# Optimization experiments

Measured on AMD Instinct MI355X. Metric: run time of the kernel, lower is better.

## Reference

```python
import jax, jax.numpy as jnp
import numpy as np

V, D, B, L = 100000, 64, 4096, 200

def setup_inputs() -> dict:
    key = jax.random.key(0)
    ks = jax.random.split(key, 10)
    s = 0.05  # keep activations in a sane range for sigmoid
    return {
        "item_ids": jax.random.randint(ks[0], (B,), 0, V),
        "history": jax.random.randint(ks[1], (B, L), 0, V),
        "hist_len": jax.random.randint(ks[2], (B,), 1, L + 1),
        "emb_table": jax.random.normal(ks[3], (V, D), jnp.float32) * s,
        "aW1": jax.random.normal(ks[4], (3 * D, D), jnp.float32) * s,
        "ab1": jnp.zeros((D,), jnp.float32),
        "aW2": jax.random.normal(ks[5], (D, 1), jnp.float32) * s,
        "ab2": jnp.zeros((1,), jnp.float32),
        "fW1": jax.random.normal(ks[6], (3 * D, 128), jnp.float32) * s,
        "fb1": jnp.zeros((128,), jnp.float32),
        "fW2": jax.random.normal(ks[7], (128, 64), jnp.float32) * s,
        "fb2": jnp.zeros((64,), jnp.float32),
        "fW3": jax.random.normal(ks[8], (64, 1), jnp.float32) * s,
        "fb3": jnp.zeros((1,), jnp.float32),
    }

def reference(item_ids, history, hist_len, emb_table, aW1, ab1, aW2, ab2,
              fW1, fb1, fW2, fb2, fW3, fb3):
    target = emb_table[item_ids]                      # [B, D]
    hist = emb_table[history]                         # [B, L, D]
    # original pads short histories with zero rows -> zero the padded tail
    mask = (jnp.arange(hist.shape[1])[None, :] < hist_len[:, None]).astype(hist.dtype)
    hist = hist * mask[..., None]
    tgt = jnp.broadcast_to(target[:, None, :], hist.shape)     # [B, L, D]
    # attention_fc takes 3*D features: (hist, target, hist*target)
    feat = jnp.concatenate([hist, tgt, hist * tgt], axis=-1)   # [B, L, 3D]
    h = jax.nn.relu(feat @ aW1 + ab1)                 # [B, L, D]
    scores = (h @ aW2 + ab2)[..., 0]                  # [B, L]
    # faithful to original: softmax over full padded length (no length mask)
    w = jax.nn.softmax(scores, axis=1)
    pooled = jnp.einsum('bl,bld->bd', w, hist)        # [B, D]
    comb = jnp.concatenate([target, pooled, pooled - target], axis=-1)  # [B, 3D]
    z = jax.nn.relu(comb @ fW1 + fb1)
    z = jax.nn.relu(z @ fW2 + fb2)
    return jax.nn.sigmoid(z @ fW3 + fb3)              # [B, 1]
```

## Files before the change

### kernel.cpp

```cpp
#include <hip/hip_runtime.h>
#include <hip/hip_bf16.h>

#define NV 100000
#define ND 64
#define NB 4096
#define NL 200
#define MT 13

typedef __bf16 bf16_t;
typedef __bf16 bf16x8 __attribute__((ext_vector_type(8)));
typedef __bf16 bf16x4 __attribute__((ext_vector_type(4)));
typedef float f32x4 __attribute__((ext_vector_type(4)));

#define TB_ELEMS ((long)NV * ND)
#define TBV (TB_ELEMS / 8)
#define FT1 (128 * 192)
#define FT2 (64 * 128)
#define AWT (64 * 192)
#define CVT_TASKS (TBV + FT1 + FT2 + AWT)

__global__ __launch_bounds__(256)
void cvt_kernel(const float* __restrict__ emb,
                const float* __restrict__ aW1,
                const float* __restrict__ fW1,
                const float* __restrict__ fW2,
                bf16_t* __restrict__ tb,
                bf16_t* __restrict__ fW1T,
                bf16_t* __restrict__ fW2T,
                bf16_t* __restrict__ awT)
{
    long t = (long)blockIdx.x * 256 + threadIdx.x;
    if (t >= CVT_TASKS) return;
    if (t < TBV) {
        long i = t * 8;
        f32x4 a0 = *(const f32x4*)(emb + i);
        f32x4 a1 = *(const f32x4*)(emb + i + 4);
        bf16x8 o;
#pragma unroll
        for (int j = 0; j < 4; ++j) { o[j] = (bf16_t)a0[j]; o[j + 4] = (bf16_t)a1[j]; }
        *(bf16x8*)(tb + i) = o;
    } else {
        int u = (int)(t - TBV);
        if (u < FT1) {
            int n = u / 192, k = u - n * 192;
            fW1T[u] = (bf16_t)fW1[k * 128 + n];
        } else if (u < FT1 + FT2) {
            int u2 = u - FT1;
            int n = u2 >> 7, k = u2 & 127;
            fW2T[u2] = (bf16_t)fW2[k * 64 + n];
        } else {
            int u3 = u - FT1 - FT2;
            int n = u3 / 192, k = u3 - n * 192;
            awT[u3] = (bf16_t)aW1[k * 64 + n];
        }
    }
}

__global__ __launch_bounds__(512, 4)
void din_kernel1(const int* __restrict__ item_ids,
                 const int* __restrict__ history,
                 const int* __restrict__ hist_len,
                 const float* __restrict__ emb,
                 const bf16_t* __restrict__ tb,
                 const bf16_t* __restrict__ awT,
                 const float* __restrict__ ab1,
                 const float* __restrict__ aW2,
                 const bf16_t* __restrict__ fW1T, const float* __restrict__ fb1,
                 const bf16_t* __restrict__ fW2T, const float* __restrict__ fb2,
                 const float* __restrict__ fW3, const float* __restrict__ fb3,
                 float* __restrict__ out)
{
    __shared__ __align__(16) bf16_t histA[2][208 * 64];
    __shared__ __align__(16) bf16_t wbT[2][64 * 64];
    __shared__ float tgt[2][64];
    __shared__ __align__(16) float scores[2][208];
    __shared__ float wts[2][208];
    __shared__ float pp2[2][512];
    __shared__ float red[2][8];
    __shared__ float cb2[2][64];

    bf16_t* comb16 = (bf16_t*)wbT;
    bf16_t* z1s    = (bf16_t*)wbT + 3200;
    float*  z2f    = (float*)((bf16_t*)wbT + 5376);

    const int b0  = blockIdx.x * 2;
    const int tid = threadIdx.x;
    const int len0 = hist_len[b0];
    const int len1 = hist_len[b0 + 1];

    if (tid < 128) {
        int bx = tid >> 6, d = tid & 63;
        tgt[bx][d] = emb[(long)item_ids[b0 + bx] * ND + d];
    }

    {
        const int p = tid & 1;
        const int s = tid >> 1;
        const int bxA = (s >= 208);
        const int lA  = s - bxA * 208;
        const int lB  = s + 48;
        const int lenA = bxA ? len1 : len0;
        const bool vB = (s < 160);
        const bf16x8 z = (bf16x8)(bf16_t)0.f;
        bf16x8 a0 = z, a1 = z, a2 = z, a3 = z;
        bf16x8 c0 = z, c1 = z, c2 = z, c3 = z;
        if (lA < lenA) {
            const bf16_t* src = tb + (long)history[(long)(b0 + bxA) * NL + lA] * ND + p * 32;
            a0 = *(const bf16x8*)(src);
            a1 = *(const bf16x8*)(src + 8);
            a2 = *(const bf16x8*)(src + 16);
            a3 = *(const bf16x8*)(src + 24);
        }
        if (vB && lB < len1) {
            const bf16_t* src = tb + (long)history[(long)(b0 + 1) * NL + lB] * ND + p * 32;
            c0 = *(const bf16x8*)(src);
            c1 = *(const bf16x8*)(src + 8);
            c2 = *(const bf16x8*)(src + 16);
            c3 = *(const bf16x8*)(src + 24);
        }
        {
            bf16_t* d = &histA[bxA][lA * 64];
            const int S = (lA & 7) << 3;
            *(bf16x8*)&d[(p * 32 +  0) ^ S] = a0;
            *(bf16x8*)&d[(p * 32 +  8) ^ S] = a1;
            *(bf16x8*)&d[(p * 32 + 16) ^ S] = a2;
            *(bf16x8*)&d[(p * 32 + 24) ^ S] = a3;
        }
        if (vB) {
            bf16_t* d = &histA[1][lB * 64];
            const int S = (lB & 7) << 3;
            *(bf16x8*)&d[(p * 32 +  0) ^ S] = c0;
            *(bf16x8*)&d[(p * 32 +  8) ^ S] = c1;
            *(bf16x8*)&d[(p * 32 + 16) ^ S] = c2;
            *(bf16x8*)&d[(p * 32 + 24) ^ S] = c3;
        }
    }

    {
        const int n  = tid & 63;
        const int kp = tid >> 6;
        const long t0 = (long)item_ids[b0] * ND;
        const long t1 = (long)item_ids[b0 + 1] * ND;
        f32x4 tk0a = *(const f32x4*)(emb + t0 + kp * 8);
        f32x4 tk0b = *(const f32x4*)(emb + t0 + kp * 8 + 4);
        f32x4 tk1a = *(const f32x4*)(emb + t1 + kp * 8);
        f32x4 tk1b = *(const f32x4*)(emb + t1 + kp * 8 + 4);
        bf16x8 va = *(const bf16x8*)&awT[n * 192 + kp * 8];
        bf16x8 vm = *(const bf16x8*)&awT[n * 192 + 64 + kp * 8];
        bf16x8 vp = *(const bf16x8*)&awT[n * 192 + 128 + kp * 8];
        float cs0 = 0.f, cs1 = 0.f;
        bf16x8 w0v, w1v;
#pragma unroll
        for (int i = 0; i < 8; ++i) {
            float tk0 = (i < 4) ? tk0a[i] : tk0b[i - 4];
            float tk1 = (i < 4) ? tk1a[i] : tk1b[i - 4];
            float ah = (float)va[i];
            float am = (float)vm[i];
            float ap = (float)vp[i];
            w0v[i] = (bf16_t)(ah + tk0 * ap);
            w1v[i] = (bf16_t)(ah + tk1 * ap);
            cs0 += tk0 * am;
            cs1 += tk1 * am;
        }
        const int S = (n & 7) << 3;
        *(bf16x8*)&wbT[0][n * 64 + ((kp * 8) ^ S)] = w0v;
        *(bf16x8*)&wbT[1][n * 64 + ((kp * 8) ^ S)] = w1v;
        pp2[0][kp * 64 + n] = cs0;
        pp2[1][kp * 64 + n] = cs1;
    }
    __syncthreads();

    if (tid < 128) {
        const int bx = tid >> 6, n = tid & 63;
        float s = ab1[n];
#pragma unroll
        for (int kp = 0; kp < 8; ++kp) s += pp2[bx][kp * 64 + n];
        cb2[bx][n] = s;
    }
    __syncthreads();

    {
        const int wave = tid >> 6;
        const int lane = tid & 63;
        const int bx   = wave & 1;
        const int col  = lane & 15;
        const int quad = lane >> 4;

        bf16x8 afrag[4][2];
#pragma unroll
        for (int nt = 0; nt < 4; ++nt) {
            const int n = nt * 16 + col;
            const int S = (n & 7) << 3;
#pragma unroll
            for (int kb = 0; kb < 2; ++kb)
                afrag[nt][kb] = *(const bf16x8*)&wbT[bx][n * 64 + ((kb * 32 + quad * 8) ^ S)];
        }
        float cv[4][4], a2[4][4];
#pragma unroll
        for (int nt = 0; nt < 4; ++nt)
#pragma unroll
            for (int i = 0; i < 4; ++i) {
                const int no = nt * 16 + quad * 4 + i;
                cv[nt][i] = cb2[bx][no];
                a2[nt][i] = aW2[no];
            }

        for (int mt = (wave >> 1); mt < MT; mt += 4) {
            const int l = mt * 16 + col;
            const int S = (l & 7) << 3;
            const bf16_t* base = &histA[bx][l * 64];
            bf16x8 bf0 = *(const bf16x8*)&base[(     quad * 8) ^ S];
            bf16x8 bf1 = *(const bf16x8*)&base[(32 + quad * 8) ^ S];
            float sc = 0.f;
#pragma unroll
            for (int nt = 0; nt < 4; ++nt) {
                f32x4 acc = {cv[nt][0], cv[nt][1], cv[nt][2], cv[nt][3]};
                acc = __builtin_amdgcn_mfma_f32_16x16x32_bf16(afrag[nt][0], bf0, acc, 0, 0, 0);
                acc = __builtin_amdgcn_mfma_f32_16x16x32_bf16(afrag[nt][1], bf1, acc, 0, 0, 0);
#pragma unroll
                for (int i = 0; i < 4; ++i) {
                    float h = acc[i] > 0.f ? acc[i] : 0.f;
                    sc += h * a2[nt][i];
                }
            }
            sc += __shfl_xor(sc, 16, 64);
            sc += __shfl_xor(sc, 32, 64);
            if (quad == 0) scores[bx][mt * 16 + col] = sc;
        }
    }
    __syncthreads();

    {
        const int bx = tid >> 8, t = tid & 255;
        float s = (t < NL) ? scores[bx][t] : -1e30f;
        float m = s;
        for (int off = 32; off > 0; off >>= 1) m = fmaxf(m, __shfl_xor(m, off, 64));
        float e = (t < NL) ? __expf(s - m) : 0.f;
        if (t < NL) wts[bx][t] = e;
        else if (t < 208) wts[bx][t] = 0.f;
        float ss = e;
        for (int off = 32; off > 0; off >>= 1) ss += __shfl_xor(ss, off, 64);
        if ((t & 63) == 0) { red[bx][t >> 6] = m; red[bx][4 + (t >> 6)] = ss; }
    }
    __syncthreads();

    {
        const int bx = tid >> 8, t = tid & 255;
        const int c = t & 15;
        const int g = t >> 4;
        const int w4 = (tid >> 6) & 3;
        const float m0 = red[bx][0], m1 = red[bx][1], m2 = red[bx][2], m3 = red[bx][3];
        const float mg = fmaxf(fmaxf(m0, m1), fmaxf(m2, m3));
        float sc0 = __expf(m0 - mg), sc1 = __expf(m1 - mg);
        float sc2 = __expf(m2 - mg), sc3 = __expf(m3 - mg);
        const float rtot = 1.f / (sc0 * red[bx][4] + sc1 * red[bx][5] +
                                  sc2 * red[bx][6] + sc3 * red[bx][7]);
        sc0 *= rtot; sc1 *= rtot; sc2 *= rtot; sc3 *= rtot;
        f32x4 acc = {0.f, 0.f, 0.f, 0.f};
#pragma unroll
        for (int j = 0; j < 13; ++j) {
            const int l = g + j * 16;
            const float scj = (j < 4) ? sc0 : (j < 8) ? sc1 : (j < 12) ? sc2 : sc3;
            const float wl = wts[bx][l] * scj;
            bf16x4 v = *(const bf16x4*)&histA[bx][l * 64 + ((c * 4) ^ ((l & 7) << 3))];
#pragma unroll
            for (int k = 0; k < 4; ++k) acc[k] += wl * (float)v[k];
        }
#pragma unroll
        for (int k = 0; k < 4; ++k) {
            acc[k] += __shfl_xor(acc[k], 16, 64);
            acc[k] += __shfl_xor(acc[k], 32, 64);
        }
        if ((tid & 63) < 16) *(f32x4*)&pp2[bx][w4 * 64 + c * 4] = acc;
    }

    bf16x8 bw1[6]; float b1v;
    bf16x8 bw2[4]; float b2v = 0.f;
    {
        const int wave = tid >> 6, lane = tid & 63;
        const int col = lane & 15, quad = lane >> 4;
        const int n = wave * 16 + col;
#pragma unroll
        for (int ks = 0; ks < 6; ++ks)
            bw1[ks] = *(const bf16x8*)&fW1T[(long)n * 192 + ks * 32 + quad * 8];
        b1v = fb1[n];
        if (wave < 4) {
            const int n2 = wave * 16 + col;
#pragma unroll
            for (int ks = 0; ks < 4; ++ks)
                bw2[ks] = *(const bf16x8*)&fW2T[(long)n2 * 128 + ks * 32 + quad * 8];
            b2v = fb2[n2];
        }
    }
    __syncthreads();

    {
        const int bx = tid >> 8, t = tid & 255;
        if (t < 192) {
            const int d = t & 63;
            float v;
            if (t < 64) v = tgt[bx][d];
            else {
                float pl = pp2[bx][d] + pp2[bx][64 + d] + pp2[bx][128 + d] + pp2[bx][192 + d];
                v = (t < 128) ? pl : pl - tgt[bx][d];
            }
            comb16[bx * 200 + t] = (bf16_t)v;
        }
        if (tid >= 384) {
            const bf16x8 z = (bf16x8)(bf16_t)0.f;
            const int u = tid - 384;
#pragma unroll
            for (int s = u; s < 350; s += 128) *(bf16x8*)&comb16[400 + s * 8] = z;
        }
    }
    __syncthreads();

    {
        const int wave = tid >> 6, lane = tid & 63;
        const int col = lane & 15, quad = lane >> 4;
        f32x4 acc = {b1v, b1v, b1v, b1v};
#pragma unroll
        for (int ks = 0; ks < 6; ++ks) {
            bf16x8 a = *(const bf16x8*)&comb16[col * 200 + ks * 32 + quad * 8];
            acc = __builtin_amdgcn_mfma_f32_16x16x32_bf16(a, bw1[ks], acc, 0, 0, 0);
        }
        const int n = wave * 16 + col;
#pragma unroll
        for (int i = 0; i < 4; ++i) {
            const int m = quad * 4 + i;
            float zv = (m < 2) ? fmaxf(acc[i], 0.f) : 0.f;
            z1s[m * 136 + n] = (bf16_t)zv;
        }
    }
    __syncthreads();

    {
        const int wave = tid >> 6, lane = tid & 63;
        const int col = lane & 15, quad = lane >> 4;
        if (wave < 4) {
            f32x4 acc = {b2v, b2v, b2v, b2v};
#pragma unroll
            for (int ks = 0; ks < 4; ++ks) {
                bf16x8 a = *(const bf16x8*)&z1s[col * 136 + ks * 32 + quad * 8];
                acc = __builtin_amdgcn_mfma_f32_16x16x32_bf16(a, bw2[ks], acc, 0, 0, 0);
            }
            const int n2 = wave * 16 + col;
#pragma unroll
            for (int i = 0; i < 4; ++i) {
                const int m = quad * 4 + i;
                if (m < 2) z2f[m * 64 + n2] = fmaxf(acc[i], 0.f);
            }
        }
    }
    __syncthreads();

    if (tid < 128) {
        const int bx = tid >> 6, j = tid & 63;
        float s = z2f[bx * 64 + j] * fW3[j];
        for (int off = 32; off > 0; off >>= 1) s += __shfl_xor(s, off, 64);
        if (j == 0) out[b0 + bx] = 1.f / (1.f + __expf(-(s + fb3[0])));
    }
}

extern "C" void kernel_launch(void* const* d_in, const int* in_sizes, int n_in,
                              void* d_out, int out_size, void* d_ws, size_t ws_size,
                              hipStream_t stream) {
    const int*   item_ids = (const int*)d_in[0];
    const int*   history  = (const int*)d_in[1];
    const int*   hist_len = (const int*)d_in[2];
    const float* emb      = (const float*)d_in[3];
    const float* aW1      = (const float*)d_in[4];
    const float* ab1      = (const float*)d_in[5];
    const float* aW2      = (const float*)d_in[6];
    const float* fW1      = (const float*)d_in[8];
    const float* fb1      = (const float*)d_in[9];
    const float* fW2      = (const float*)d_in[10];
    const float* fb2      = (const float*)d_in[11];
    const float* fW3      = (const float*)d_in[12];
    const float* fb3      = (const float*)d_in[13];

    bf16_t* tb   = (bf16_t*)d_ws;
    bf16_t* fW1T = tb + TB_ELEMS;
    bf16_t* fW2T = fW1T + FT1;
    bf16_t* awTp = fW2T + FT2;

    cvt_kernel<<<(int)((CVT_TASKS + 255) / 256), 256, 0, stream>>>(
        emb, aW1, fW1, fW2, tb, fW1T, fW2T, awTp);
    din_kernel1<<<NB / 2, 512, 0, stream>>>(item_ids, history, hist_len, emb, tb,
                                            awTp, ab1, aW2,
                                            fW1T, fb1, fW2T, fb2, fW3, fb3,
                                            (float*)d_out);
}
```

Before: 145.1 us.

## Restructure target-weight folding, drop padding zeroing, and hoist MLP weight loads

The folded attention-weight setup now gives each wave a single batch element and reduces the target-dependent bias with wave shuffles. This removes the shared-memory partial-sum pass and one block barrier. aW1 is converted to bf16 without a transpose, so the conversion writes are coalesced, and the kernel reads it row-wise. The fW1/fW2 register loads are moved ahead of the pooling step so their latency overlaps it. The zero-fill of unused comb16/z1s rows is removed, so those MFMA rows hold stale data whose results are then discarded.

```diff
diff --git a/kernel.cpp b/kernel.cpp
--- a/kernel.cpp
+++ b/kernel.cpp
@@ -16,8 +16,8 @@
 #define TBV (TB_ELEMS / 8)
 #define FT1 (128 * 192)
 #define FT2 (64 * 128)
-#define AWT (64 * 192)
-#define CVT_TASKS (TBV + FT1 + FT2 + AWT)
+#define AWB (192 * 64)
+#define CVT_TASKS (TBV + FT1 + FT2 + AWB)
 
 __global__ __launch_bounds__(256)
 void cvt_kernel(const float* __restrict__ emb,
@@ -27,7 +27,7 @@
                 bf16_t* __restrict__ tb,
                 bf16_t* __restrict__ fW1T,
                 bf16_t* __restrict__ fW2T,
-                bf16_t* __restrict__ awT)
+                bf16_t* __restrict__ awB)
 {
     long t = (long)blockIdx.x * 256 + threadIdx.x;
     if (t >= CVT_TASKS) return;
@@ -50,8 +50,7 @@
             fW2T[u2] = (bf16_t)fW2[k * 64 + n];
         } else {
             int u3 = u - FT1 - FT2;
-            int n = u3 / 192, k = u3 - n * 192;
-            awT[u3] = (bf16_t)aW1[k * 64 + n];
+            awB[u3] = (bf16_t)aW1[u3];
         }
     }
 }
@@ -62,7 +61,8 @@
                  const int* __restrict__ hist_len,
                  const float* __restrict__ emb,
                  const bf16_t* __restrict__ tb,
-                 const bf16_t* __restrict__ awT,
+                 const float* __restrict__ aW1,
+                 const bf16_t* __restrict__ awB,
                  const float* __restrict__ ab1,
                  const float* __restrict__ aW2,
                  const bf16_t* __restrict__ fW1T, const float* __restrict__ fb1,
@@ -75,7 +75,7 @@
     __shared__ float tgt[2][64];
     __shared__ __align__(16) float scores[2][208];
     __shared__ float wts[2][208];
-    __shared__ float pp2[2][512];
+    __shared__ float pp2[2][256];
     __shared__ float red[2][8];
     __shared__ float cb2[2][64];
 
@@ -137,45 +137,36 @@
     }
 
     {
-        const int n  = tid & 63;
-        const int kp = tid >> 6;
-        const long t0 = (long)item_ids[b0] * ND;
-        const long t1 = (long)item_ids[b0 + 1] * ND;
-        f32x4 tk0a = *(const f32x4*)(emb + t0 + kp * 8);
-        f32x4 tk0b = *(const f32x4*)(emb + t0 + kp * 8 + 4);
-        f32x4 tk1a = *(const f32x4*)(emb + t1 + kp * 8);
-        f32x4 tk1b = *(const f32x4*)(emb + t1 + kp * 8 + 4);
-        bf16x8 va = *(const bf16x8*)&awT[n * 192 + kp * 8];
-        bf16x8 vm = *(const bf16x8*)&awT[n * 192 + 64 + kp * 8];
-        bf16x8 vp = *(const bf16x8*)&awT[n * 192 + 128 + kp * 8];
-        float cs0 = 0.f, cs1 = 0.f;
+        const int lane = tid & 63;
+        const int w    = tid >> 6;
+        const int bx   = w & 1;
+        const int n    = ((w >> 1) << 4) | (lane & 15);
+        const int kq   = lane >> 4;
+        const long t0  = (long)item_ids[b0 + bx] * ND;
+        f32x4 tka = *(const f32x4*)(emb + t0 + kq * 16);
+        f32x4 tkb = *(const f32x4*)(emb + t0 + kq * 16 + 4);
+        f32x4 tkc = *(const f32x4*)(emb + t0 + kq * 16 + 8);
+        f32x4 tkd = *(const f32x4*)(emb + t0 + kq * 16 + 12);
+        float csum = 0.f;
         bf16x8 w0v, w1v;
 #pragma unroll
-        for (int i = 0; i < 8; ++i) {
-            float tk0 = (i < 4) ? tk0a[i] : tk0b[i - 4];
-            float tk1 = (i < 4) ? tk1a[i] : tk1b[i - 4];
-            float ah = (float)va[i];
-            float am = (float)vm[i];
-            float ap = (float)vp[i];
-            w0v[i] = (bf16_t)(ah + tk0 * ap);
-            w1v[i] = (bf16_t)(ah + tk1 * ap);
-            cs0 += tk0 * am;
-            cs1 += tk1 * am;
+        for (int i = 0; i < 16; ++i) {
+            int k = kq * 16 + i;
+            float tk = (i < 4) ? tka[i] : (i < 8) ? tkb[i - 4]
+                     : (i < 12) ? tkc[i - 8] : tkd[i - 12];
+            float ah = (float)awB[k * 64 + n];
+            float am = aW1[(64 + k) * 64 + n];
+            float ap = (float)awB[(128 + k) * 64 + n];
+            float wv = ah + tk * ap;
+            if (i < 8) w0v[i] = (bf16_t)wv; else w1v[i - 8] = (bf16_t)wv;
+            csum += tk * am;
         }
         const int S = (n & 7) << 3;
-        *(bf16x8*)&wbT[0][n * 64 + ((kp * 8) ^ S)] = w0v;
-        *(bf16x8*)&wbT[1][n * 64 + ((kp * 8) ^ S)] = w1v;
-        pp2[0][kp * 64 + n] = cs0;
-        pp2[1][kp * 64 + n] = cs1;
-    }
-    __syncthreads();
-
-    if (tid < 128) {
-        const int bx = tid >> 6, n = tid & 63;
-        float s = ab1[n];
-#pragma unroll
-        for (int kp = 0; kp < 8; ++kp) s += pp2[bx][kp * 64 + n];
-        cb2[bx][n] = s;
+        *(bf16x8*)&wbT[bx][n * 64 + ((kq * 16    ) ^ S)] = w0v;
+        *(bf16x8*)&wbT[bx][n * 64 + ((kq * 16 + 8) ^ S)] = w1v;
+        csum += __shfl_xor(csum, 16, 64);
+        csum += __shfl_xor(csum, 32, 64);
+        if (kq == 0) cb2[bx][n] = ab1[n] + csum;
     }
     __syncthreads();
 
@@ -243,6 +234,25 @@
         if ((t & 63) == 0) { red[bx][t >> 6] = m; red[bx][4 + (t >> 6)] = ss; }
     }
     __syncthreads();
+
+    bf16x8 bw1[6]; float b1v;
+    bf16x8 bw2[4]; float b2v = 0.f;
+    {
+        const int wave = tid >> 6, lane = tid & 63;
+        const int col = lane & 15, quad = lane >> 4;
+        const int n = wave * 16 + col;
+#pragma unroll
+        for (int ks = 0; ks < 6; ++ks)
+            bw1[ks] = *(const bf16x8*)&fW1T[(long)n * 192 + ks * 32 + quad * 8];
+        b1v = fb1[n];
+        if (wave < 4) {
+            const int n2 = wave * 16 + col;
+#pragma unroll
+            for (int ks = 0; ks < 4; ++ks)
+                bw2[ks] = *(const bf16x8*)&fW2T[(long)n2 * 128 + ks * 32 + quad * 8];
+            b2v = fb2[n2];
+        }
+    }
 
     {
         const int bx = tid >> 8, t = tid & 255;
@@ -273,25 +283,6 @@
         }
         if ((tid & 63) < 16) *(f32x4*)&pp2[bx][w4 * 64 + c * 4] = acc;
     }
-
-    bf16x8 bw1[6]; float b1v;
-    bf16x8 bw2[4]; float b2v = 0.f;
-    {
-        const int wave = tid >> 6, lane = tid & 63;
-        const int col = lane & 15, quad = lane >> 4;
-        const int n = wave * 16 + col;
-#pragma unroll
-        for (int ks = 0; ks < 6; ++ks)
-            bw1[ks] = *(const bf16x8*)&fW1T[(long)n * 192 + ks * 32 + quad * 8];
-        b1v = fb1[n];
-        if (wave < 4) {
-            const int n2 = wave * 16 + col;
-#pragma unroll
-            for (int ks = 0; ks < 4; ++ks)
-                bw2[ks] = *(const bf16x8*)&fW2T[(long)n2 * 128 + ks * 32 + quad * 8];
-            b2v = fb2[n2];
-        }
-    }
     __syncthreads();
 
     {
@@ -306,12 +297,6 @@
             }
             comb16[bx * 200 + t] = (bf16_t)v;
         }
-        if (tid >= 384) {
-            const bf16x8 z = (bf16x8)(bf16_t)0.f;
-            const int u = tid - 384;
-#pragma unroll
-            for (int s = u; s < 350; s += 128) *(bf16x8*)&comb16[400 + s * 8] = z;
-        }
     }
     __syncthreads();
 
@@ -328,8 +313,7 @@
 #pragma unroll
         for (int i = 0; i < 4; ++i) {
             const int m = quad * 4 + i;
-            float zv = (m < 2) ? fmaxf(acc[i], 0.f) : 0.f;
-            z1s[m * 136 + n] = (bf16_t)zv;
+            if (m < 2) z1s[m * 136 + n] = (bf16_t)fmaxf(acc[i], 0.f);
         }
     }
     __syncthreads();
@@ -382,12 +366,12 @@
     bf16_t* tb   = (bf16_t*)d_ws;
     bf16_t* fW1T = tb + TB_ELEMS;
     bf16_t* fW2T = fW1T + FT1;
-    bf16_t* awTp = fW2T + FT2;
+    bf16_t* awBp = fW2T + FT2;
 
     cvt_kernel<<<(int)((CVT_TASKS + 255) / 256), 256, 0, stream>>>(
-        emb, aW1, fW1, fW2, tb, fW1T, fW2T, awTp);
+        emb, aW1, fW1, fW2, tb, fW1T, fW2T, awBp);
     din_kernel1<<<NB / 2, 512, 0, stream>>>(item_ids, history, hist_len, emb, tb,
-                                            awTp, ab1, aW2,
+                                            aW1, awBp, ab1, aW2,
                                             fW1T, fb1, fW2T, fb2, fW3, fb3,
                                             (float*)d_out);
 }
```

New measurement: 141.8 us. 2.3% less time.
